# Kernel tuning notes

Measured on AMD Instinct MI355X. Metric: run time of the kernel, lower is better.

Reference implementation:

```python
import jax, jax.numpy as jnp
import numpy as np
import math

HIDDEN = 1024
INTER = 4096
HEADS = 16
HEAD_DIM = 64
INNER = HEADS * HEAD_DIM
SEQ = 4096


def setup_inputs() -> dict:
    key = jax.random.key(0)
    ks = jax.random.split(key, 16)
    s = 0.02
    d = dict(
        x=jax.random.normal(ks[0], (SEQ, HIDDEN), dtype=jnp.float32),
        # attention norm
        an_w=jnp.ones((HIDDEN,), jnp.float32),
        an_b=jnp.zeros((HIDDEN,), jnp.float32),
        # attention projections (weight stored as [out, in] like torch)
        q_w=jax.random.normal(ks[1], (INNER, HIDDEN)) * s,
        q_b=jnp.zeros((INNER,), jnp.float32),
        k_w=jax.random.normal(ks[2], (INNER, HIDDEN)) * s,
        k_b=jnp.zeros((INNER,), jnp.float32),
        v_w=jax.random.normal(ks[3], (INNER, HIDDEN)) * s,
        v_b=jnp.zeros((INNER,), jnp.float32),
        o_w=jax.random.normal(ks[4], (HIDDEN, INNER)) * s,
        o_b=jnp.zeros((HIDDEN,), jnp.float32),
        # ff norm
        fn_w=jnp.ones((HIDDEN,), jnp.float32),
        fn_b=jnp.zeros((HIDDEN,), jnp.float32),
        ff1_w=jax.random.normal(ks[5], (INTER, HIDDEN)) * s,
        ff1_b=jnp.zeros((INTER,), jnp.float32),
        ff2_w=jax.random.normal(ks[6], (HIDDEN, INTER)) * s,
        ff2_b=jnp.zeros((HIDDEN,), jnp.float32),
    )
    return d


def _norm_novar(x, w, b):
    # mean-only layer norm (no variance normalization)
    return w * (x - jnp.mean(x, axis=-1, keepdims=True)) + b


def _block(x, an_w, an_b, q_w, q_b, k_w, k_b, v_w, v_b, o_w, o_b,
           fn_w, fn_b, ff1_w, ff1_b, ff2_w, ff2_b):
    S = x.shape[0]
    scale = math.sqrt(HEAD_DIM)
    xn = _norm_novar(x, an_w, an_b)
    # [S, inner] -> [h, S, d]
    Q = (xn @ q_w.T + q_b).reshape(S, HEADS, HEAD_DIM).transpose(1, 0, 2)
    K = (xn @ k_w.T + k_b).reshape(S, HEADS, HEAD_DIM).transpose(1, 0, 2)
    V = (xn @ v_w.T + v_b).reshape(S, HEADS, HEAD_DIM).transpose(1, 0, 2)
    scores = jnp.einsum('hsd,htd->hst', Q, K) / scale  # [h, S, S]
    attn = jax.nn.softmax(scores, axis=-1)
    ctx = jnp.einsum('hst,htd->hsd', attn, V)  # [h, S, d]
    ctx = ctx.transpose(1, 0, 2).reshape(S, INNER)
    x = ctx @ o_w.T + o_b + x
    xn = _norm_novar(x, fn_w, fn_b)
    h = jax.nn.relu(xn @ ff1_w.T + ff1_b)
    return h @ ff2_w.T + ff2_b + x


def reference(x, an_w, an_b, q_w, q_b, k_w, k_b, v_w, v_b, o_w, o_b,
              fn_w, fn_b, ff1_w, ff1_b, ff2_w, ff2_b):
    return _block(x, an_w, an_b, q_w, q_b, k_w, k_b, v_w, v_b, o_w, o_b,
                  fn_w, fn_b, ff1_w, ff1_b, ff2_w, ff2_b)
```

## Files before the change

### kernel.cpp

```cpp
#include <hip/hip_runtime.h>
#include <hip/hip_bf16.h>

#define SQ 4096
#define HID 1024
#define INTER_DIM 4096
#define NH 16
#define DH 64

typedef __attribute__((ext_vector_type(4))) float f32x4;
typedef __attribute__((ext_vector_type(16))) float f32x16;
typedef __attribute__((ext_vector_type(8))) short bf16x8;

__device__ __forceinline__ unsigned short f2bf(float f) {
  union { float f; unsigned int i; } v; v.f = f;
  unsigned int i = v.i;
  return (unsigned short)((i + 0x7FFFu + ((i >> 16) & 1u)) >> 16);
}

__device__ __forceinline__ void load_lds16(const void* g, void* l) {
  __builtin_amdgcn_global_load_lds(
      (const __attribute__((address_space(1))) void*)g,
      (__attribute__((address_space(3))) void*)l, 16, 0, 0);
}

__device__ __forceinline__ int cvtpk_bf16(float a, float b) {
  int r;
  asm("v_cvt_pk_bf16_f32 %0, %1, %2" : "=v"(r) : "v"(a), "v"(b));
  return r;
}

__global__ __launch_bounds__(256) void cvt6_kernel(
    const float* __restrict__ s0, const float* __restrict__ s1,
    const float* __restrict__ s2, const float* __restrict__ s3,
    const float* __restrict__ s4, const float* __restrict__ s5,
    unsigned short* __restrict__ dst) {
  const int b = blockIdx.x;
  const float* src;
  int lb;
  size_t base4;
  if (b < 4096) {
    const int r = b >> 10;
    lb = b & 1023;
    src = (r == 0) ? s0 : (r == 1) ? s1 : (r == 2) ? s2 : s3;
    base4 = (size_t)r << 18;
  } else if (b < 8192) {
    lb = b - 4096; src = s4; base4 = 1u << 20;
  } else {
    lb = b - 8192; src = s5; base4 = 2u << 20;
  }
  const int i = lb * 256 + threadIdx.x;
  const float4 v4 = ((const float4*)src)[i];
  ushort4 o4;
  o4.x = f2bf(v4.x); o4.y = f2bf(v4.y); o4.z = f2bf(v4.z); o4.w = f2bf(v4.w);
  ((ushort4*)dst)[base4 + i] = o4;
}

__global__ __launch_bounds__(256) void ln_kernel(
    const float* __restrict__ x, const float* __restrict__ w,
    const float* __restrict__ b, unsigned short* __restrict__ out) {
  const int row = blockIdx.x;
  const int t = threadIdx.x;
  const float4 v = ((const float4*)(x + (size_t)row * HID))[t];
  float s = v.x + v.y + v.z + v.w;
  #pragma unroll
  for (int off = 32; off > 0; off >>= 1) s += __shfl_xor(s, off);
  __shared__ float red[4];
  if ((t & 63) == 0) red[t >> 6] = s;
  __syncthreads();
  const float mean = (red[0] + red[1] + red[2] + red[3]) * (1.0f / HID);
  const float4 wv = ((const float4*)w)[t];
  const float4 bv = ((const float4*)b)[t];
  ushort4 o;
  o.x = f2bf(wv.x * (v.x - mean) + bv.x);
  o.y = f2bf(wv.y * (v.y - mean) + bv.y);
  o.z = f2bf(wv.z * (v.z - mean) + bv.z);
  o.w = f2bf(wv.w * (v.w - mean) + bv.w);
  ((ushort4*)(out + (size_t)row * HID))[t] = o;
}

template <int MODE>
__global__ __launch_bounds__(256) void gemm_bt(
    const unsigned short* __restrict__ A, const unsigned short* __restrict__ B,
    const float* __restrict__ bias, const float* __restrict__ res,
    void* __restrict__ Cout, int M, int N, int K, float scale) {
  __shared__ __align__(16) unsigned short As[128 * 32];
  __shared__ __align__(16) unsigned short Bs[128 * 32];
  const int t = threadIdx.x;
  const int lane = t & 63;
  const int wave = t >> 6;
  const int g = lane >> 4;
  const int lr = lane & 15;
  const int waveM = wave >> 1, waveN = wave & 1;
  const int rowBase = blockIdx.x * 128;
  const int colBase = blockIdx.y * 128;

  f32x4 acc[4][4];
  #pragma unroll
  for (int m = 0; m < 4; ++m)
    #pragma unroll
    for (int n = 0; n < 4; ++n) acc[m][n] = (f32x4){0.f, 0.f, 0.f, 0.f};

  const int c0 = t, c1 = t + 256;
  const int r0s = c0 >> 2, s0 = (c0 & 3) ^ (r0s & 3);
  const int r1s = c1 >> 2, s1 = (c1 & 3) ^ (r1s & 3);
  const unsigned short* gA0 = A + (size_t)(rowBase + r0s) * K + s0 * 8;
  const unsigned short* gA1 = A + (size_t)(rowBase + r1s) * K + s1 * 8;
  const unsigned short* gB0 = B + (size_t)(colBase + r0s) * K + s0 * 8;
  const unsigned short* gB1 = B + (size_t)(colBase + r1s) * K + s1 * 8;
  unsigned short* lA0 = &As[wave * 512];
  unsigned short* lA1 = &As[2048 + wave * 512];
  unsigned short* lB0 = &Bs[wave * 512];
  unsigned short* lB1 = &Bs[2048 + wave * 512];

  for (int k0 = 0; k0 < K; k0 += 32) {
    load_lds16(gA0 + k0, lA0);
    load_lds16(gA1 + k0, lA1);
    load_lds16(gB0 + k0, lB0);
    load_lds16(gB1 + k0, lB1);
    __syncthreads();
    bf16x8 af[4], bfr[4];
    #pragma unroll
    for (int m = 0; m < 4; ++m) {
      int r = waveM * 64 + m * 16 + lr;
      af[m] = *(const bf16x8*)&As[r * 32 + ((g ^ (r & 3)) << 3)];
    }
    #pragma unroll
    for (int n = 0; n < 4; ++n) {
      int c = waveN * 64 + n * 16 + lr;
      bfr[n] = *(const bf16x8*)&Bs[c * 32 + ((g ^ (c & 3)) << 3)];
    }
    #pragma unroll
    for (int m = 0; m < 4; ++m)
      #pragma unroll
      for (int n = 0; n < 4; ++n)
        acc[m][n] = __builtin_amdgcn_mfma_f32_16x16x32_bf16(af[m], bfr[n],
                                                            acc[m][n], 0, 0, 0);
    __syncthreads();
  }

  const int crow0 = rowBase + waveM * 64;
  const int ccol0 = colBase + waveN * 64;
  #pragma unroll
  for (int n = 0; n < 4; ++n) {
    const int col = ccol0 + n * 16 + lr;
    const float bv = bias[col];
    #pragma unroll
    for (int m = 0; m < 4; ++m) {
      if (MODE == 3) {
        const int row0 = crow0 + m * 16 + g * 4;
        ushort4 o4;
        o4.x = f2bf(acc[m][n][0] + bv);
        o4.y = f2bf(acc[m][n][1] + bv);
        o4.z = f2bf(acc[m][n][2] + bv);
        o4.w = f2bf(acc[m][n][3] + bv);
        *(ushort4*)&((unsigned short*)Cout)[(size_t)col * M + row0] = o4;
      } else {
        #pragma unroll
        for (int j = 0; j < 4; ++j) {
          const int row = crow0 + m * 16 + g * 4 + j;
          const float v = acc[m][n][j] + bv;
          if (MODE == 0) {
            ((unsigned short*)Cout)[(size_t)row * N + col] = f2bf(v * scale);
          } else if (MODE == 1) {
            ((unsigned short*)Cout)[(size_t)row * N + col] = f2bf(fmaxf(v, 0.f));
          } else {
            ((float*)Cout)[(size_t)row * N + col] =
                v + res[(size_t)row * N + col];
          }
        }
      }
    }
  }
}

__global__ __launch_bounds__(256, 2) void attn_kernel(
    const unsigned short* __restrict__ Q,
    const unsigned short* __restrict__ Kg,
    const unsigned short* __restrict__ Vt,
    unsigned short* __restrict__ ctx) {
  const int s = blockIdx.y * gridDim.x + blockIdx.x;
  const int q6 = s >> 3;
  const int h = (s & 7) * 2 + (q6 >> 5);
  const int qt = q6 & 31;

  const int t = threadIdx.x;
  const int lane = t & 63;
  const int wave = t >> 6;
  const int ql = lane & 31;
  const int hi = lane >> 5;

  __shared__ __align__(16) unsigned short Ks[2][64 * 64];
  __shared__ __align__(16) unsigned short Vs[2][64 * 64];

  const int qbase = qt * 128 + wave * 32;
  const unsigned short* qptr = Q + (size_t)(qbase + ql) * HID + h * DH + hi * 8;
  bf16x8 qf[4];
  #pragma unroll
  for (int ks = 0; ks < 4; ++ks) qf[ks] = *(const bf16x8*)(qptr + ks * 16);

  const int cr = t >> 3, cs = t & 7;
  const int cr2 = cr + 32;
  const unsigned short* gK0 = Kg + (size_t)cr * HID + h * DH + ((cs ^ (cr & 7)) << 3);
  const unsigned short* gK1 = Kg + (size_t)cr2 * HID + h * DH + ((cs ^ (cr2 & 7)) << 3);
  const unsigned short* gV0 = Vt + (size_t)(h * DH + cr) * SQ + ((cs ^ (cr & 7)) << 3);
  const unsigned short* gV1 = Vt + (size_t)(h * DH + cr2) * SQ + ((cs ^ (cr2 & 7)) << 3);

  float mreg = -1e30f, lreg = 0.f;
  f32x16 oacc0 = 0.f, oacc1 = 0.f;

  load_lds16(gK0, &Ks[0][wave * 512]);
  load_lds16(gK1, &Ks[0][2048 + wave * 512]);
  load_lds16(gV0, &Vs[0][wave * 512]);
  load_lds16(gV1, &Vs[0][2048 + wave * 512]);

  for (int kt = 0; kt < SQ / 64; ++kt) {
    const int buf = kt & 1;
    __syncthreads();
    if (kt + 1 < SQ / 64) {
      const size_t ko = (size_t)(kt + 1) * 64 * HID;
      const int vo = (kt + 1) * 64;
      load_lds16(gK0 + ko, &Ks[buf ^ 1][wave * 512]);
      load_lds16(gK1 + ko, &Ks[buf ^ 1][2048 + wave * 512]);
      load_lds16(gV0 + vo, &Vs[buf ^ 1][wave * 512]);
      load_lds16(gV1 + vo, &Vs[buf ^ 1][2048 + wave * 512]);
    }
    const unsigned short* KsB = &Ks[buf][0];
    const unsigned short* VsB = &Vs[buf][0];

    f32x16 st0 = 0.f, st1 = 0.f;
    #pragma unroll
    for (int ks = 0; ks < 4; ++ks) {
      const int sl = ((((ks << 1) | hi) ^ (ql & 7)) << 3);
      const bf16x8 k0 = *(const bf16x8*)&KsB[ql * 64 + sl];
      const bf16x8 k1 = *(const bf16x8*)&KsB[(32 + ql) * 64 + sl];
      st0 = __builtin_amdgcn_mfma_f32_32x32x16_bf16(k0, qf[ks], st0, 0, 0, 0);
      st1 = __builtin_amdgcn_mfma_f32_32x32x16_bf16(k1, qf[ks], st1, 0, 0, 0);
    }

    bf16x8 vf0[4], vf1[4];
    #pragma unroll
    for (int ks = 0; ks < 4; ++ks) {
      const int sl = ((((ks << 1) | hi) ^ (ql & 7)) << 3);
      vf0[ks] = *(const bf16x8*)&VsB[ql * 64 + sl];
      vf1[ks] = *(const bf16x8*)&VsB[(32 + ql) * 64 + sl];
    }

    float mx = st0[0];
    #pragma unroll
    for (int r = 1; r < 16; ++r) mx = fmaxf(mx, st0[r]);
    #pragma unroll
    for (int r = 0; r < 16; ++r) mx = fmaxf(mx, st1[r]);
    mx = fmaxf(mx, __shfl_xor(mx, 32));

    if (!__all(mx <= mreg + 11.0f)) {
      const float mn = fmaxf(mreg, mx);
      const float corr = exp2f(mreg - mn);
      mreg = mn;
      lreg *= corr;
      #pragma unroll
      for (int r = 0; r < 16; ++r) {
        const float c = __shfl(corr, (r & 3) + 8 * (r >> 2) + 4 * hi);
        oacc0[r] *= c;
        oacc1[r] *= c;
      }
    }

    float sum = 0.f;
    #pragma unroll
    for (int r = 0; r < 16; ++r) { st0[r] = exp2f(st0[r] - mreg); sum += st0[r]; }
    #pragma unroll
    for (int r = 0; r < 16; ++r) { st1[r] = exp2f(st1[r] - mreg); sum += st1[r]; }
    sum += __shfl_xor(sum, 32);
    lreg += sum;

    union { int w[4]; bf16x8 v; } pa[4];
    #pragma unroll
    for (int half = 0; half < 2; ++half) {
      #pragma unroll
      for (int kk = 0; kk < 2; ++kk) {
        const int base = kk * 8;
        float p0, p1, p2, p3, p4, p5, p6, p7;
        if (half == 0) {
          p0 = st0[base + 0]; p1 = st0[base + 1]; p2 = st0[base + 2]; p3 = st0[base + 3];
          p4 = st0[base + 4]; p5 = st0[base + 5]; p6 = st0[base + 6]; p7 = st0[base + 7];
        } else {
          p0 = st1[base + 0]; p1 = st1[base + 1]; p2 = st1[base + 2]; p3 = st1[base + 3];
          p4 = st1[base + 4]; p5 = st1[base + 5]; p6 = st1[base + 6]; p7 = st1[base + 7];
        }
        const int d0 = cvtpk_bf16(p0, p1), s0 = cvtpk_bf16(p4, p5);
        const int d1 = cvtpk_bf16(p2, p3), s1 = cvtpk_bf16(p6, p7);
        auto a = __builtin_amdgcn_permlane32_swap(d0, s0, false, false);
        auto b = __builtin_amdgcn_permlane32_swap(d1, s1, false, false);
        const int ks = half * 2 + kk;
        pa[ks].w[0] = a[0]; pa[ks].w[1] = b[0];
        pa[ks].w[2] = a[1]; pa[ks].w[3] = b[1];
      }
    }

    #pragma unroll
    for (int ks = 0; ks < 4; ++ks) {
      oacc0 = __builtin_amdgcn_mfma_f32_32x32x16_bf16(pa[ks].v, vf0[ks], oacc0, 0, 0, 0);
      oacc1 = __builtin_amdgcn_mfma_f32_32x32x16_bf16(pa[ks].v, vf1[ks], oacc1, 0, 0, 0);
    }
  }

  const float linv = 1.0f / lreg;
  #pragma unroll
  for (int r = 0; r < 16; ++r) {
    const int qq = (r & 3) + 8 * (r >> 2) + 4 * hi;
    const float li = __shfl(linv, qq);
    unsigned short* cp = ctx + (size_t)(qbase + qq) * HID + h * DH + ql;
    cp[0] = f2bf(oacc0[r] * li);
    cp[32] = f2bf(oacc1[r] * li);
  }
}

extern "C" void kernel_launch(void* const* d_in, const int* in_sizes, int n_in,
                              void* d_out, int out_size, void* d_ws,
                              size_t ws_size, hipStream_t stream) {
  const float* x     = (const float*)d_in[0];
  const float* an_w  = (const float*)d_in[1];
  const float* an_b  = (const float*)d_in[2];
  const float* q_w   = (const float*)d_in[3];
  const float* q_b   = (const float*)d_in[4];
  const float* k_w   = (const float*)d_in[5];
  const float* k_b   = (const float*)d_in[6];
  const float* v_w   = (const float*)d_in[7];
  const float* v_b   = (const float*)d_in[8];
  const float* o_w   = (const float*)d_in[9];
  const float* o_b   = (const float*)d_in[10];
  const float* fn_w  = (const float*)d_in[11];
  const float* fn_b  = (const float*)d_in[12];
  const float* ff1_w = (const float*)d_in[13];
  const float* ff1_b = (const float*)d_in[14];
  const float* ff2_w = (const float*)d_in[15];
  const float* ff2_b = (const float*)d_in[16];

  char* ws = (char*)d_ws;
  const size_t MB = 1ull << 20;
  unsigned short* xn   = (unsigned short*)(ws + 0);
  unsigned short* qwb  = (unsigned short*)(ws + 8 * MB);
  unsigned short* kwb  = (unsigned short*)(ws + 10 * MB);
  unsigned short* vwb  = (unsigned short*)(ws + 12 * MB);
  unsigned short* owb  = (unsigned short*)(ws + 14 * MB);
  unsigned short* f1wb = (unsigned short*)(ws + 16 * MB);
  unsigned short* f2wb = (unsigned short*)(ws + 24 * MB);
  unsigned short* Qm   = (unsigned short*)(ws + 32 * MB);
  unsigned short* Km   = (unsigned short*)(ws + 40 * MB);
  unsigned short* Vtm  = (unsigned short*)(ws + 48 * MB);
  unsigned short* ctx  = (unsigned short*)(ws + 56 * MB);
  float*          x2   = (float*)(ws + 64 * MB);
  unsigned short* hbuf = (unsigned short*)(ws + 32 * MB);
  unsigned short* x2n  = xn;

  cvt6_kernel<<<12288, 256, 0, stream>>>(q_w, k_w, v_w, o_w, ff1_w, ff2_w, qwb);

  ln_kernel<<<SQ, 256, 0, stream>>>(x, an_w, an_b, xn);

  dim3 g1(SQ / 128, HID / 128);
  gemm_bt<0><<<g1, 256, 0, stream>>>(xn, qwb, q_b, nullptr, Qm, SQ, HID, HID,
                                     0.125f * 1.44269504f);
  gemm_bt<0><<<g1, 256, 0, stream>>>(xn, kwb, k_b, nullptr, Km, SQ, HID, HID, 1.0f);
  gemm_bt<3><<<g1, 256, 0, stream>>>(xn, vwb, v_b, nullptr, Vtm, SQ, HID, HID, 1.0f);

  attn_kernel<<<dim3(32, 16), 256, 0, stream>>>(Qm, Km, Vtm, ctx);

  gemm_bt<2><<<g1, 256, 0, stream>>>(ctx, owb, o_b, x, x2, SQ, HID, HID, 1.0f);

  ln_kernel<<<SQ, 256, 0, stream>>>(x2, fn_w, fn_b, x2n);

  dim3 g2(SQ / 128, INTER_DIM / 128);
  gemm_bt<1><<<g2, 256, 0, stream>>>(x2n, f1wb, ff1_b, nullptr, hbuf, SQ,
                                     INTER_DIM, HID, 1.0f);

  gemm_bt<2><<<g1, 256, 0, stream>>>(hbuf, f2wb, ff2_b, x2, (float*)d_out, SQ,
                                     HID, INTER_DIM, 1.0f);
}
```

Before: 504.7 us.

## Fuse QKV GEMM, double-buffer GEMM LDS, and streamline attention softmax

The Q, K and V projections are merged into one GEMM with N=3072. It writes Q and K interleaved into one row-major buffer and V transposed into a second buffer. The softmax scale is folded into the Q weights and bias at conversion time. The generic GEMM gains double-buffered LDS so the next K-tile load overlaps the current MFMA work. The attention kernel seeds score accumulators with the negated running max, uses tree reductions for max and sum, applies a fixed-threshold lazy rescale, and raises wave priority around MFMA blocks. Together these aim to cut launch count, reuse the A tile across the three projections, hide load latency and trim VALU work in softmax. The costs are twice the LDS in the GEMM, which can lower occupancy, and a looser overflow margin in softmax.

```diff
diff --git a/kernel.cpp b/kernel.cpp
--- a/kernel.cpp
+++ b/kernel.cpp
@@ -6,6 +6,7 @@
 #define INTER_DIM 4096
 #define NH 16
 #define DH 64
+#define SCALE_Q 0.18033688f
 
 typedef __attribute__((ext_vector_type(4))) float f32x4;
 typedef __attribute__((ext_vector_type(16))) float f32x16;
@@ -48,11 +49,23 @@
   } else {
     lb = b - 8192; src = s5; base4 = 2u << 20;
   }
+  const float sc = (b < 1024) ? SCALE_Q : 1.0f;
   const int i = lb * 256 + threadIdx.x;
   const float4 v4 = ((const float4*)src)[i];
   ushort4 o4;
-  o4.x = f2bf(v4.x); o4.y = f2bf(v4.y); o4.z = f2bf(v4.z); o4.w = f2bf(v4.w);
+  o4.x = f2bf(v4.x * sc); o4.y = f2bf(v4.y * sc);
+  o4.z = f2bf(v4.z * sc); o4.w = f2bf(v4.w * sc);
   ((ushort4*)dst)[base4 + i] = o4;
+}
+
+__global__ __launch_bounds__(256) void bias3_kernel(
+    const float* __restrict__ qb, const float* __restrict__ kb,
+    const float* __restrict__ vb, float* __restrict__ dst) {
+  const int b = blockIdx.x, t = threadIdx.x;
+  const float* s = (b == 0) ? qb : (b == 1) ? kb : vb;
+  float4 v = ((const float4*)s)[t];
+  if (b == 0) { v.x *= SCALE_Q; v.y *= SCALE_Q; v.z *= SCALE_Q; v.w *= SCALE_Q; }
+  ((float4*)dst)[b * 256 + t] = v;
 }
 
 __global__ __launch_bounds__(256) void ln_kernel(
@@ -82,9 +95,9 @@
 __global__ __launch_bounds__(256) void gemm_bt(
     const unsigned short* __restrict__ A, const unsigned short* __restrict__ B,
     const float* __restrict__ bias, const float* __restrict__ res,
-    void* __restrict__ Cout, int M, int N, int K, float scale) {
-  __shared__ __align__(16) unsigned short As[128 * 32];
-  __shared__ __align__(16) unsigned short Bs[128 * 32];
+    void* __restrict__ Cout, void* __restrict__ Cout2, int M, int N, int K) {
+  __shared__ __align__(16) unsigned short As[2][128 * 32];
+  __shared__ __align__(16) unsigned short Bs[2][128 * 32];
   const int t = threadIdx.x;
   const int lane = t & 63;
   const int wave = t >> 6;
@@ -107,27 +120,33 @@
   const unsigned short* gA1 = A + (size_t)(rowBase + r1s) * K + s1 * 8;
   const unsigned short* gB0 = B + (size_t)(colBase + r0s) * K + s0 * 8;
   const unsigned short* gB1 = B + (size_t)(colBase + r1s) * K + s1 * 8;
-  unsigned short* lA0 = &As[wave * 512];
-  unsigned short* lA1 = &As[2048 + wave * 512];
-  unsigned short* lB0 = &Bs[wave * 512];
-  unsigned short* lB1 = &Bs[2048 + wave * 512];
-
-  for (int k0 = 0; k0 < K; k0 += 32) {
-    load_lds16(gA0 + k0, lA0);
-    load_lds16(gA1 + k0, lA1);
-    load_lds16(gB0 + k0, lB0);
-    load_lds16(gB1 + k0, lB1);
-    __syncthreads();
+
+  load_lds16(gA0, &As[0][wave * 512]);
+  load_lds16(gA1, &As[0][2048 + wave * 512]);
+  load_lds16(gB0, &Bs[0][wave * 512]);
+  load_lds16(gB1, &Bs[0][2048 + wave * 512]);
+  __syncthreads();
+
+  const int nk = K >> 5;
+  for (int kt = 0; kt < nk; ++kt) {
+    const int buf = kt & 1;
+    if (kt + 1 < nk) {
+      const int k0 = (kt + 1) << 5;
+      load_lds16(gA0 + k0, &As[buf ^ 1][wave * 512]);
+      load_lds16(gA1 + k0, &As[buf ^ 1][2048 + wave * 512]);
+      load_lds16(gB0 + k0, &Bs[buf ^ 1][wave * 512]);
+      load_lds16(gB1 + k0, &Bs[buf ^ 1][2048 + wave * 512]);
+    }
     bf16x8 af[4], bfr[4];
     #pragma unroll
     for (int m = 0; m < 4; ++m) {
-      int r = waveM * 64 + m * 16 + lr;
-      af[m] = *(const bf16x8*)&As[r * 32 + ((g ^ (r & 3)) << 3)];
+      const int r = waveM * 64 + m * 16 + lr;
+      af[m] = *(const bf16x8*)&As[buf][r * 32 + ((g ^ (r & 3)) << 3)];
     }
     #pragma unroll
     for (int n = 0; n < 4; ++n) {
-      int c = waveN * 64 + n * 16 + lr;
-      bfr[n] = *(const bf16x8*)&Bs[c * 32 + ((g ^ (c & 3)) << 3)];
+      const int c = waveN * 64 + n * 16 + lr;
+      bfr[n] = *(const bf16x8*)&Bs[buf][c * 32 + ((g ^ (c & 3)) << 3)];
     }
     #pragma unroll
     for (int m = 0; m < 4; ++m)
@@ -146,36 +165,38 @@
     const float bv = bias[col];
     #pragma unroll
     for (int m = 0; m < 4; ++m) {
-      if (MODE == 3) {
-        const int row0 = crow0 + m * 16 + g * 4;
-        ushort4 o4;
-        o4.x = f2bf(acc[m][n][0] + bv);
-        o4.y = f2bf(acc[m][n][1] + bv);
-        o4.z = f2bf(acc[m][n][2] + bv);
-        o4.w = f2bf(acc[m][n][3] + bv);
-        *(ushort4*)&((unsigned short*)Cout)[(size_t)col * M + row0] = o4;
+      const int row0 = crow0 + m * 16 + g * 4;
+      if (MODE == 4) {
+        if (col < 2048) {
+          #pragma unroll
+          for (int j = 0; j < 4; ++j)
+            ((unsigned short*)Cout)[(size_t)(row0 + j) * 2048 + col] =
+                f2bf(acc[m][n][j] + bv);
+        } else {
+          ushort4 o4;
+          o4.x = f2bf(acc[m][n][0] + bv);
+          o4.y = f2bf(acc[m][n][1] + bv);
+          o4.z = f2bf(acc[m][n][2] + bv);
+          o4.w = f2bf(acc[m][n][3] + bv);
+          *(ushort4*)&((unsigned short*)Cout2)[(size_t)(col - 2048) * M + row0] = o4;
+        }
+      } else if (MODE == 1) {
+        #pragma unroll
+        for (int j = 0; j < 4; ++j)
+          ((unsigned short*)Cout)[(size_t)(row0 + j) * N + col] =
+              f2bf(fmaxf(acc[m][n][j] + bv, 0.f));
       } else {
         #pragma unroll
-        for (int j = 0; j < 4; ++j) {
-          const int row = crow0 + m * 16 + g * 4 + j;
-          const float v = acc[m][n][j] + bv;
-          if (MODE == 0) {
-            ((unsigned short*)Cout)[(size_t)row * N + col] = f2bf(v * scale);
-          } else if (MODE == 1) {
-            ((unsigned short*)Cout)[(size_t)row * N + col] = f2bf(fmaxf(v, 0.f));
-          } else {
-            ((float*)Cout)[(size_t)row * N + col] =
-                v + res[(size_t)row * N + col];
-          }
-        }
+        for (int j = 0; j < 4; ++j)
+          ((float*)Cout)[(size_t)(row0 + j) * N + col] =
+              acc[m][n][j] + bv + res[(size_t)(row0 + j) * N + col];
       }
     }
   }
 }
 
 __global__ __launch_bounds__(256, 2) void attn_kernel(
-    const unsigned short* __restrict__ Q,
-    const unsigned short* __restrict__ Kg,
+    const unsigned short* __restrict__ QK,
     const unsigned short* __restrict__ Vt,
     unsigned short* __restrict__ ctx) {
   const int s = blockIdx.y * gridDim.x + blockIdx.x;
@@ -193,19 +214,22 @@
   __shared__ __align__(16) unsigned short Vs[2][64 * 64];
 
   const int qbase = qt * 128 + wave * 32;
-  const unsigned short* qptr = Q + (size_t)(qbase + ql) * HID + h * DH + hi * 8;
+  const unsigned short* qptr =
+      QK + (size_t)(qbase + ql) * 2048 + h * DH + hi * 8;
   bf16x8 qf[4];
   #pragma unroll
   for (int ks = 0; ks < 4; ++ks) qf[ks] = *(const bf16x8*)(qptr + ks * 16);
 
   const int cr = t >> 3, cs = t & 7;
   const int cr2 = cr + 32;
-  const unsigned short* gK0 = Kg + (size_t)cr * HID + h * DH + ((cs ^ (cr & 7)) << 3);
-  const unsigned short* gK1 = Kg + (size_t)cr2 * HID + h * DH + ((cs ^ (cr2 & 7)) << 3);
+  const unsigned short* gK0 =
+      QK + (size_t)cr * 2048 + 1024 + h * DH + ((cs ^ (cr & 7)) << 3);
+  const unsigned short* gK1 =
+      QK + (size_t)cr2 * 2048 + 1024 + h * DH + ((cs ^ (cr2 & 7)) << 3);
   const unsigned short* gV0 = Vt + (size_t)(h * DH + cr) * SQ + ((cs ^ (cr & 7)) << 3);
   const unsigned short* gV1 = Vt + (size_t)(h * DH + cr2) * SQ + ((cs ^ (cr2 & 7)) << 3);
 
-  float mreg = -1e30f, lreg = 0.f;
+  float mreg = 0.f, lreg = 0.f;
   f32x16 oacc0 = 0.f, oacc1 = 0.f;
 
   load_lds16(gK0, &Ks[0][wave * 512]);
@@ -217,7 +241,7 @@
     const int buf = kt & 1;
     __syncthreads();
     if (kt + 1 < SQ / 64) {
-      const size_t ko = (size_t)(kt + 1) * 64 * HID;
+      const size_t ko = (size_t)(kt + 1) * 64 * 2048;
       const int vo = (kt + 1) * 64;
       load_lds16(gK0 + ko, &Ks[buf ^ 1][wave * 512]);
       load_lds16(gK1 + ko, &Ks[buf ^ 1][2048 + wave * 512]);
@@ -227,7 +251,10 @@
     const unsigned short* KsB = &Ks[buf][0];
     const unsigned short* VsB = &Vs[buf][0];
 
-    f32x16 st0 = 0.f, st1 = 0.f;
+    f32x16 st0, st1;
+    #pragma unroll
+    for (int r = 0; r < 16; ++r) { st0[r] = -mreg; st1[r] = -mreg; }
+    __builtin_amdgcn_s_setprio(1);
     #pragma unroll
     for (int ks = 0; ks < 4; ++ks) {
       const int sl = ((((ks << 1) | hi) ^ (ql & 7)) << 3);
@@ -236,6 +263,7 @@
       st0 = __builtin_amdgcn_mfma_f32_32x32x16_bf16(k0, qf[ks], st0, 0, 0, 0);
       st1 = __builtin_amdgcn_mfma_f32_32x32x16_bf16(k1, qf[ks], st1, 0, 0, 0);
     }
+    __builtin_amdgcn_s_setprio(0);
 
     bf16x8 vf0[4], vf1[4];
     #pragma unroll
@@ -245,18 +273,22 @@
       vf1[ks] = *(const bf16x8*)&VsB[(32 + ql) * 64 + sl];
     }
 
-    float mx = st0[0];
-    #pragma unroll
-    for (int r = 1; r < 16; ++r) mx = fmaxf(mx, st0[r]);
-    #pragma unroll
-    for (int r = 0; r < 16; ++r) mx = fmaxf(mx, st1[r]);
-    mx = fmaxf(mx, __shfl_xor(mx, 32));
-
-    if (!__all(mx <= mreg + 11.0f)) {
-      const float mn = fmaxf(mreg, mx);
-      const float corr = exp2f(mreg - mn);
-      mreg = mn;
+    float tr[16];
+    #pragma unroll
+    for (int r = 0; r < 16; ++r) tr[r] = fmaxf(st0[r], st1[r]);
+    #pragma unroll
+    for (int s2 = 8; s2 > 0; s2 >>= 1)
+      #pragma unroll
+      for (int r = 0; r < s2; ++r) tr[r] = fmaxf(tr[r], tr[r + s2]);
+    const float mx = fmaxf(tr[0], __shfl_xor(tr[0], 32));
+
+    if (!__all(mx <= 8.0f)) {
+      const float mpos = fmaxf(mx, 0.f);
+      const float corr = exp2f(-mpos);
+      mreg += mpos;
       lreg *= corr;
+      #pragma unroll
+      for (int r = 0; r < 16; ++r) { st0[r] -= mpos; st1[r] -= mpos; }
       #pragma unroll
       for (int r = 0; r < 16; ++r) {
         const float c = __shfl(corr, (r & 3) + 8 * (r >> 2) + 4 * hi);
@@ -265,13 +297,18 @@
       }
     }
 
-    float sum = 0.f;
-    #pragma unroll
-    for (int r = 0; r < 16; ++r) { st0[r] = exp2f(st0[r] - mreg); sum += st0[r]; }
-    #pragma unroll
-    for (int r = 0; r < 16; ++r) { st1[r] = exp2f(st1[r] - mreg); sum += st1[r]; }
-    sum += __shfl_xor(sum, 32);
-    lreg += sum;
+    #pragma unroll
+    for (int r = 0; r < 16; ++r) st0[r] = exp2f(st0[r]);
+    #pragma unroll
+    for (int r = 0; r < 16; ++r) st1[r] = exp2f(st1[r]);
+    float ts[16];
+    #pragma unroll
+    for (int r = 0; r < 16; ++r) ts[r] = st0[r] + st1[r];
+    #pragma unroll
+    for (int s2 = 8; s2 > 0; s2 >>= 1)
+      #pragma unroll
+      for (int r = 0; r < s2; ++r) ts[r] += ts[r + s2];
+    lreg += ts[0] + __shfl_xor(ts[0], 32);
 
     union { int w[4]; bf16x8 v; } pa[4];
     #pragma unroll
@@ -287,21 +324,23 @@
           p0 = st1[base + 0]; p1 = st1[base + 1]; p2 = st1[base + 2]; p3 = st1[base + 3];
           p4 = st1[base + 4]; p5 = st1[base + 5]; p6 = st1[base + 6]; p7 = st1[base + 7];
         }
-        const int d0 = cvtpk_bf16(p0, p1), s0 = cvtpk_bf16(p4, p5);
-        const int d1 = cvtpk_bf16(p2, p3), s1 = cvtpk_bf16(p6, p7);
-        auto a = __builtin_amdgcn_permlane32_swap(d0, s0, false, false);
-        auto b = __builtin_amdgcn_permlane32_swap(d1, s1, false, false);
+        const int d0 = cvtpk_bf16(p0, p1), sw0 = cvtpk_bf16(p4, p5);
+        const int d1 = cvtpk_bf16(p2, p3), sw1 = cvtpk_bf16(p6, p7);
+        auto a = __builtin_amdgcn_permlane32_swap(d0, sw0, false, false);
+        auto b = __builtin_amdgcn_permlane32_swap(d1, sw1, false, false);
         const int ks = half * 2 + kk;
         pa[ks].w[0] = a[0]; pa[ks].w[1] = b[0];
         pa[ks].w[2] = a[1]; pa[ks].w[3] = b[1];
       }
     }
 
+    __builtin_amdgcn_s_setprio(1);
     #pragma unroll
     for (int ks = 0; ks < 4; ++ks) {
       oacc0 = __builtin_amdgcn_mfma_f32_32x32x16_bf16(pa[ks].v, vf0[ks], oacc0, 0, 0, 0);
       oacc1 = __builtin_amdgcn_mfma_f32_32x32x16_bf16(pa[ks].v, vf1[ks], oacc1, 0, 0, 0);
     }
+    __builtin_amdgcn_s_setprio(0);
   }
 
   const float linv = 1.0f / lreg;
@@ -338,41 +377,37 @@
 
   char* ws = (char*)d_ws;
   const size_t MB = 1ull << 20;
-  unsigned short* xn   = (unsigned short*)(ws + 0);
-  unsigned short* qwb  = (unsigned short*)(ws + 8 * MB);
-  unsigned short* kwb  = (unsigned short*)(ws + 10 * MB);
-  unsigned short* vwb  = (unsigned short*)(ws + 12 * MB);
-  unsigned short* owb  = (unsigned short*)(ws + 14 * MB);
-  unsigned short* f1wb = (unsigned short*)(ws + 16 * MB);
-  unsigned short* f2wb = (unsigned short*)(ws + 24 * MB);
-  unsigned short* Qm   = (unsigned short*)(ws + 32 * MB);
-  unsigned short* Km   = (unsigned short*)(ws + 40 * MB);
-  unsigned short* Vtm  = (unsigned short*)(ws + 48 * MB);
-  unsigned short* ctx  = (unsigned short*)(ws + 56 * MB);
-  float*          x2   = (float*)(ws + 64 * MB);
-  unsigned short* hbuf = (unsigned short*)(ws + 32 * MB);
-  unsigned short* x2n  = xn;
-
-  cvt6_kernel<<<12288, 256, 0, stream>>>(q_w, k_w, v_w, o_w, ff1_w, ff2_w, qwb);
+  unsigned short* xn    = (unsigned short*)(ws + 0);
+  unsigned short* qkvwb = (unsigned short*)(ws + 8 * MB);
+  unsigned short* owb   = (unsigned short*)(ws + 14 * MB);
+  unsigned short* f1wb  = (unsigned short*)(ws + 16 * MB);
+  unsigned short* f2wb  = (unsigned short*)(ws + 24 * MB);
+  unsigned short* QKm   = (unsigned short*)(ws + 32 * MB);
+  unsigned short* Vtm   = (unsigned short*)(ws + 48 * MB);
+  unsigned short* ctx   = (unsigned short*)(ws + 56 * MB);
+  float*          bAll  = (float*)(ws + 56 * MB);
+  float*          x2    = (float*)(ws + 64 * MB);
+  unsigned short* hbuf  = (unsigned short*)(ws + 32 * MB);
+  unsigned short* x2n   = xn;
+
+  cvt6_kernel<<<12288, 256, 0, stream>>>(q_w, k_w, v_w, o_w, ff1_w, ff2_w, qkvwb);
+  bias3_kernel<<<3, 256, 0, stream>>>(q_b, k_b, v_b, bAll);
 
   ln_kernel<<<SQ, 256, 0, stream>>>(x, an_w, an_b, xn);
 
-  dim3 g1(SQ / 128, HID / 128);
-  gemm_bt<0><<<g1, 256, 0, stream>>>(xn, qwb, q_b, nullptr, Qm, SQ, HID, HID,
-                                     0.125f * 1.44269504f);
-  gemm_bt<0><<<g1, 256, 0, stream>>>(xn, kwb, k_b, nullptr, Km, SQ, HID, HID, 1.0f);
-  gemm_bt<3><<<g1, 256, 0, stream>>>(xn, vwb, v_b, nullptr, Vtm, SQ, HID, HID, 1.0f);
-
-  attn_kernel<<<dim3(32, 16), 256, 0, stream>>>(Qm, Km, Vtm, ctx);
-
-  gemm_bt<2><<<g1, 256, 0, stream>>>(ctx, owb, o_b, x, x2, SQ, HID, HID, 1.0f);
+  gemm_bt<4><<<dim3(SQ / 128, 3072 / 128), 256, 0, stream>>>(
+      xn, qkvwb, bAll, nullptr, QKm, Vtm, SQ, 3072, HID);
+
+  attn_kernel<<<dim3(32, 16), 256, 0, stream>>>(QKm, Vtm, ctx);
+
+  gemm_bt<2><<<dim3(SQ / 128, HID / 128), 256, 0, stream>>>(
+      ctx, owb, o_b, x, x2, nullptr, SQ, HID, HID);
 
   ln_kernel<<<SQ, 256, 0, stream>>>(x2, fn_w, fn_b, x2n);
 
-  dim3 g2(SQ / 128, INTER_DIM / 128);
-  gemm_bt<1><<<g2, 256, 0, stream>>>(x2n, f1wb, ff1_b, nullptr, hbuf, SQ,
-                                     INTER_DIM, HID, 1.0f);
-
-  gemm_bt<2><<<g1, 256, 0, stream>>>(hbuf, f2wb, ff2_b, x2, (float*)d_out, SQ,
-                                     HID, INTER_DIM, 1.0f);
-}
+  gemm_bt<1><<<dim3(SQ / 128, INTER_DIM / 128), 256, 0, stream>>>(
+      x2n, f1wb, ff1_b, nullptr, hbuf, nullptr, SQ, INTER_DIM, HID);
+
+  gemm_bt<2><<<dim3(SQ / 128, HID / 128), 256, 0, stream>>>(
+      hbuf, f2wb, ff2_b, x2, (float*)d_out, nullptr, SQ, HID, INTER_DIM);
+}
```

Result: faster. 446.7 us (-11.5%).
